# Kernel tuning notes

Measured on AMD Instinct MI355X. Metric: run time of the kernel, lower is better.

## Reference

```python
import jax, jax.numpy as jnp
import numpy as np

NUM_CLASSES = 40
EOS_COEF = 0.1
IGNORE = 255
W_CLASS, W_MASK, W_DICE = 2.0, 5.0, 5.0
EPS = 1e-8


def setup_inputs() -> dict:
    key = jax.random.key(0)
    k1, k2, k3, k4 = jax.random.split(key, 4)
    B, Q, H, W = 4, 100, 256, 256
    pred_logits = jax.random.normal(k1, (B, Q, NUM_CLASSES + 1), dtype=jnp.float32)
    pred_masks = jax.random.normal(k2, (B, Q, H, W), dtype=jnp.float32)
    targets = jax.random.randint(k3, (B, H, W), 0, NUM_CLASSES)
    ign = jax.random.uniform(k4, (B, H, W)) < 0.05
    targets = jnp.where(ign, IGNORE, targets).astype(jnp.int32)
    return {"pred_logits": pred_logits, "pred_masks": pred_masks, "targets": targets}


def reference(pred_logits, pred_masks, targets):
    B, Q, _ = pred_logits.shape
    C = NUM_CLASSES
    f32 = jnp.float32
    valid = targets != IGNORE                      # [B,H,W]
    tgt_safe = jnp.where(valid, targets, 0)        # in-range for indexing

    # ---- loss_labels: pixel->query assignment, per-query mode label ----
    # sigmoid is monotone, so argmax over queries of raw logits == argmax of sigmoid
    assign = jnp.argmax(pred_masks, axis=1)        # [B,H,W]
    b_idx = jnp.broadcast_to(jnp.arange(B)[:, None, None], targets.shape)
    # counts[b,q,c] = #valid pixels assigned to query q with label c
    counts = jnp.zeros((B, Q, C), f32).at[b_idx, assign, tgt_safe].add(valid.astype(f32))
    has_pix = counts.sum(-1) > 0                   # [B,Q]
    # mode = argmax of counts (ties -> smallest class, matching torch.mode)
    target_classes = jnp.where(has_pix, jnp.argmax(counts, axis=-1), C)  # [B,Q]

    logp = jax.nn.log_softmax(pred_logits, axis=-1)                      # [B,Q,C+1]
    nll = -jnp.take_along_axis(logp, target_classes[..., None], axis=-1)[..., 0]
    empty_weight = jnp.ones(C + 1, f32).at[-1].set(EOS_COEF)
    # ignore_index = num_classes in the CE over classes
    ce = jnp.where(target_classes != C, nll * empty_weight[target_classes], 0.0)
    p = jnp.exp(-ce)
    loss_ce = jnp.mean((1.0 - p) ** 2 * ce)

    # ---- loss_masks: per-pixel CE over queries + per-class dice ----
    logp_pix = jax.nn.log_softmax(pred_masks, axis=1)                    # [B,Q,H,W]
    nll_pix = -jnp.take_along_axis(logp_pix, tgt_safe[:, None], axis=1)[:, 0]  # [B,H,W]
    n_valid = valid.astype(f32).sum()
    ce_mask = jnp.sum(jnp.where(valid, nll_pix, 0.0)) / jnp.maximum(n_valid, 1.0)

    sig = jax.nn.sigmoid(pred_masks)                                     # [B,Q,H,W]
    tmask = (targets[:, None] == jnp.arange(C)[None, :, None, None]).astype(f32)  # [B,C,H,W]
    vm = valid[:, None].astype(f32)                                      # [B,1,H,W]
    inter = jnp.einsum('bqhw,bchw->bqc', sig, tmask * vm)                # numerator uses valid mask
    src_sum = sig.sum(axis=(2, 3))                                       # [B,Q]
    tsum = tmask.sum(axis=(2, 3))                                        # [B,C]
    dice = 2.0 * inter / (src_sum[:, :, None] + tsum[:, None, :] + EPS)  # [B,Q,C]
    present = tsum.sum(axis=0) > 0                                       # [C]
    dice_loss = jnp.sum(jnp.where(present, 1.0 - dice.mean(axis=(0, 1)), 0.0)) / C

    combined = W_MASK * ce_mask + W_DICE * dice_loss
    return W_CLASS * loss_ce + combined
```

## Files before the change

kernel.cpp:

```cpp
#include <hip/hip_runtime.h>
#include <hip/hip_bf16.h>

constexpr int B = 4, Q = 100, C = 40, Cp1 = 41, HW = 65536;
constexpr int NPIX = B * HW;

constexpr int APXT = 4, ATHR = 128;
constexpr int ABLK = NPIX / (APXT * ATHR);
constexpr int SLOT = ABLK / B;
constexpr int QU = 10;

constexpr int BTHR = 128, BCHUNKS = 8;
constexpr int BCPX = HW / BCHUNKS;
constexpr int BITERS = BCPX / (BTHR * 4);

constexpr int WS_WORDS = 32562;

__global__ void kZ(unsigned* __restrict__ ws, int n) {
    int i = blockIdx.x * blockDim.x + threadIdx.x;
    for (; i < n; i += gridDim.x * blockDim.x) ws[i] = 0u;
}

__global__ __launch_bounds__(ATHR) void kA(const float* __restrict__ masks,
                                           const int* __restrict__ targets,
                                           unsigned* __restrict__ counts,
                                           unsigned* __restrict__ tsum,
                                           float* __restrict__ ce_sum,
                                           unsigned* __restrict__ n_valid) {
    int tid = threadIdx.x;
    int blk = blockIdx.x;
    int b = blk / SLOT;
    int hw = (blk % SLOT) * (ATHR * APXT) + tid * APXT;
    const float* mp = masks + (size_t)b * Q * HW + hw;
    int4 tg = *(const int4*)(targets + (size_t)b * HW + hw);
    int tgs[4] = {tg.x, tg.y, tg.z, tg.w};

    float m[4] = {-INFINITY, -INFINITY, -INFINITY, -INFINITY};
    float s[4] = {0.f, 0.f, 0.f, 0.f};
    float xt[4] = {0.f, 0.f, 0.f, 0.f};
    int amax[4] = {0, 0, 0, 0};

    for (int qq = 0; qq < Q; qq += QU) {
        float4 vv[QU];
        #pragma unroll
        for (int u = 0; u < QU; ++u)
            vv[u] = *(const float4*)(mp + (size_t)(qq + u) * HW);
        #pragma unroll
        for (int u = 0; u < QU; ++u) {
            int q = qq + u;
            float v[4] = {vv[u].x, vv[u].y, vv[u].z, vv[u].w};
            #pragma unroll
            for (int j = 0; j < 4; ++j) {
                s[j] += __expf(v[j]);
                amax[j] = (v[j] > m[j]) ? q : amax[j];
                m[j] = fmaxf(m[j], v[j]);
                xt[j] = (q == tgs[j]) ? v[j] : xt[j];
            }
        }
    }

    __shared__ unsigned ts_local[C];
    __shared__ float cred[2];
    __shared__ unsigned vred[2];
    if (tid < C) ts_local[tid] = 0u;
    __syncthreads();

    float ce = 0.f;
    unsigned nv = 0;
    #pragma unroll
    for (int j = 0; j < 4; ++j) {
        if (tgs[j] != 255) {
            ce += __logf(s[j]) - xt[j];
            nv++;
            atomicAdd(&counts[((size_t)b * Q + amax[j]) * C + tgs[j]], 1u);
            atomicAdd(&ts_local[tgs[j]], 1u);
        }
    }

    for (int off = 32; off; off >>= 1) {
        ce += __shfl_xor(ce, off);
        nv += __shfl_xor(nv, off);
    }
    int lane = tid & 63, wave = tid >> 6;
    if (lane == 0) { cred[wave] = ce; vred[wave] = nv; }
    __syncthreads();
    if (tid == 0) {
        atomicAdd(ce_sum, cred[0] + cred[1]);
        atomicAdd(n_valid, vred[0] + vred[1]);
    }
    if (tid < C) {
        unsigned t = ts_local[tid];
        if (t) atomicAdd(&tsum[b * C + tid], t);
    }
}

__global__ __launch_bounds__(BTHR) void kB(const float* __restrict__ masks,
                                           const int* __restrict__ targets,
                                           float* __restrict__ inter,
                                           float* __restrict__ src_sum) {
    __shared__ float hist[C][BTHR];
    int tid = threadIdx.x;
    int bq = blockIdx.x >> 3;
    int chunk = blockIdx.x & 7;
    int b = bq / Q;
    const float* mp = masks + (size_t)bq * HW + chunk * BCPX;
    const int* tp = targets + (size_t)b * HW + chunk * BCPX;

    #pragma unroll
    for (int c = 0; c < C; ++c) hist[c][tid] = 0.f;

    float sacc = 0.f;
    #pragma unroll 4
    for (int it = 0; it < BITERS; ++it) {
        int off = it * (BTHR * 4) + tid * 4;
        float4 x = *(const float4*)(mp + off);
        int4 tg = *(const int4*)(tp + off);
        float xs[4] = {x.x, x.y, x.z, x.w};
        int cs[4] = {tg.x, tg.y, tg.z, tg.w};
        #pragma unroll
        for (int j = 0; j < 4; ++j) {
            float sig = __builtin_amdgcn_rcpf(1.f + __expf(-xs[j]));
            sacc += sig;
            if ((unsigned)cs[j] < (unsigned)C) hist[cs[j]][tid] += sig;
        }
    }

    for (int off = 32; off; off >>= 1) sacc += __shfl_xor(sacc, off);
    int lane = tid & 63, wave = tid >> 6;
    if (lane == 0) atomicAdd(&src_sum[bq], sacc);

    __syncthreads();
    for (int c = wave * 20; c < wave * 20 + 20; ++c) {
        float h = hist[c][lane] + hist[c][lane + 64];
        for (int off = 32; off; off >>= 1) h += __shfl_xor(h, off);
        if (lane == 0) atomicAdd(&inter[(size_t)bq * C + c], h);
    }
}

__global__ __launch_bounds__(512) void kC(const float* __restrict__ logits,
                                          const unsigned* __restrict__ counts,
                                          const unsigned* __restrict__ tsum,
                                          const float* __restrict__ inter,
                                          const float* __restrict__ src_sum,
                                          const float* __restrict__ ce_sum,
                                          const unsigned* __restrict__ n_valid,
                                          float* __restrict__ out) {
    int tid = threadIdx.x;
    __shared__ float dice_sum[C];
    __shared__ float wred[8];
    __shared__ float s_lce;
    if (tid < C) dice_sum[tid] = 0.f;

    float ce_acc = 0.f;
    for (int i = tid; i < B * Q; i += 512) {
        const unsigned* cnt = counts + (size_t)i * C;
        unsigned best = 0;
        int tc = C;
        #pragma unroll
        for (int c = 0; c < C; ++c) {
            unsigned v = cnt[c];
            if (v > best) { best = v; tc = c; }
        }
        if (tc != C) {
            const float* lg = logits + (size_t)i * Cp1;
            float mm = -INFINITY, xt = 0.f;
            #pragma unroll
            for (int c = 0; c < Cp1; ++c) {
                float v = lg[c];
                mm = fmaxf(mm, v);
                if (c == tc) xt = v;
            }
            float ss = 0.f;
            #pragma unroll
            for (int c = 0; c < Cp1; ++c) ss += __expf(lg[c] - mm);
            float nll = mm + __logf(ss) - xt;
            float p = __expf(-nll);
            float om = 1.f - p;
            ce_acc += om * om * nll;
        }
    }
    for (int off = 32; off; off >>= 1) ce_acc += __shfl_xor(ce_acc, off);
    if ((tid & 63) == 0) wred[tid >> 6] = ce_acc;
    __syncthreads();
    if (tid == 0) {
        float t = 0.f;
        for (int w = 0; w < 8; ++w) t += wred[w];
        s_lce = t;
    }

    for (int i = tid; i < B * Q * C; i += 512) {
        int bq = i / C, c = i - bq * C;
        float denom = src_sum[bq] + (float)tsum[(bq / Q) * C + c] + 1e-8f;
        atomicAdd(&dice_sum[c], 2.f * inter[i] / denom);
    }
    __syncthreads();

    if (tid == 0) {
        float dl = 0.f;
        for (int c = 0; c < C; ++c) {
            unsigned ts = tsum[c] + tsum[C + c] + tsum[2 * C + c] + tsum[3 * C + c];
            if (ts > 0) dl += 1.f - dice_sum[c] * (1.f / (B * Q));
        }
        dl *= (1.f / C);
        float ce_mask = ce_sum[0] / fmaxf((float)n_valid[0], 1.f);
        float lce = s_lce * (1.f / (B * Q));
        out[0] = 2.f * lce + 5.f * ce_mask + 5.f * dl;
    }
}

extern "C" void kernel_launch(void* const* d_in, const int* in_sizes, int n_in,
                              void* d_out, int out_size, void* d_ws, size_t ws_size,
                              hipStream_t stream) {
    const float* logits  = (const float*)d_in[0];
    const float* masks   = (const float*)d_in[1];
    const int*   targets = (const int*)d_in[2];
    float* out = (float*)d_out;

    unsigned* ws      = (unsigned*)d_ws;
    unsigned* counts  = ws;
    unsigned* tsum    = ws + 16000;
    float*    inter   = (float*)(ws + 16160);
    float*    src_sum = (float*)(ws + 32160);
    float*    ce_sum  = (float*)(ws + 32560);
    unsigned* n_valid = ws + 32561;

    kZ<<<64, 256, 0, stream>>>(ws, WS_WORDS);
    kA<<<ABLK, ATHR, 0, stream>>>(masks, targets, counts, tsum, ce_sum, n_valid);
    kB<<<B * Q * BCHUNKS, BTHR, 0, stream>>>(masks, targets, inter, src_sum);
    kC<<<1, 512, 0, stream>>>(logits, counts, tsum, inter, src_sum, ce_sum, n_valid, out);
}
```

Before: 230.8 us.

## Merge argmax/CE and dice histogram passes into one heterogeneous-block kernel

```diff
diff --git a/kernel.cpp b/kernel.cpp
--- a/kernel.cpp
+++ b/kernel.cpp
@@ -4,14 +4,16 @@
 constexpr int B = 4, Q = 100, C = 40, Cp1 = 41, HW = 65536;
 constexpr int NPIX = B * HW;
 
-constexpr int APXT = 4, ATHR = 128;
-constexpr int ABLK = NPIX / (APXT * ATHR);
-constexpr int SLOT = ABLK / B;
-constexpr int QU = 10;
-
-constexpr int BTHR = 128, BCHUNKS = 8;
-constexpr int BCPX = HW / BCHUNKS;
-constexpr int BITERS = BCPX / (BTHR * 4);
+constexpr int ATHR = 256, APX = 2;
+constexpr int ABLKS = NPIX / (ATHR * APX);
+constexpr int ASLOT = HW / (ATHR * APX);
+constexpr int QU = 5;
+
+constexpr int BCH = 8;
+constexpr int BCPX = HW / BCH;
+constexpr int BIT = BCPX / (ATHR * 4);
+
+constexpr int GRID = ABLKS + B * Q * BCH;
 
 constexpr int WS_WORDS = 32562;
 
@@ -20,119 +22,117 @@
     for (; i < n; i += gridDim.x * blockDim.x) ws[i] = 0u;
 }
 
-__global__ __launch_bounds__(ATHR) void kA(const float* __restrict__ masks,
-                                           const int* __restrict__ targets,
-                                           unsigned* __restrict__ counts,
-                                           unsigned* __restrict__ tsum,
-                                           float* __restrict__ ce_sum,
-                                           unsigned* __restrict__ n_valid) {
+__global__ __launch_bounds__(256, 4) void kBig(const float* __restrict__ masks,
+                                               const int* __restrict__ targets,
+                                               unsigned* __restrict__ counts,
+                                               unsigned* __restrict__ tsum,
+                                               float* __restrict__ ce_sum,
+                                               unsigned* __restrict__ n_valid,
+                                               float* __restrict__ inter,
+                                               float* __restrict__ src_sum) {
+    __shared__ float hist[C][ATHR];
     int tid = threadIdx.x;
     int blk = blockIdx.x;
-    int b = blk / SLOT;
-    int hw = (blk % SLOT) * (ATHR * APXT) + tid * APXT;
-    const float* mp = masks + (size_t)b * Q * HW + hw;
-    int4 tg = *(const int4*)(targets + (size_t)b * HW + hw);
-    int tgs[4] = {tg.x, tg.y, tg.z, tg.w};
-
-    float m[4] = {-INFINITY, -INFINITY, -INFINITY, -INFINITY};
-    float s[4] = {0.f, 0.f, 0.f, 0.f};
-    float xt[4] = {0.f, 0.f, 0.f, 0.f};
-    int amax[4] = {0, 0, 0, 0};
-
-    for (int qq = 0; qq < Q; qq += QU) {
-        float4 vv[QU];
+
+    if (blk < ABLKS) {
+        unsigned* ts_local = (unsigned*)&hist[0][0];
+        float*    cred     = &hist[0][64];
+        unsigned* vred     = (unsigned*)&hist[0][72];
+
+        int b = blk / ASLOT;
+        int hw = (blk % ASLOT) * (ATHR * APX) + tid * APX;
+        const float* mp = masks + (size_t)b * Q * HW + hw;
+        int2 tg = *(const int2*)(targets + (size_t)b * HW + hw);
+        int tgs[2] = {tg.x, tg.y};
+
+        float m[2] = {-INFINITY, -INFINITY}, s[2] = {0.f, 0.f}, xt[2] = {0.f, 0.f};
+        int amax[2] = {0, 0};
+
+        for (int qq = 0; qq < Q; qq += QU) {
+            float2 vv[QU];
+            #pragma unroll
+            for (int u = 0; u < QU; ++u)
+                vv[u] = *(const float2*)(mp + (size_t)(qq + u) * HW);
+            #pragma unroll
+            for (int u = 0; u < QU; ++u) {
+                int q = qq + u;
+                float v[2] = {vv[u].x, vv[u].y};
+                #pragma unroll
+                for (int j = 0; j < 2; ++j) {
+                    s[j] += __expf(v[j]);
+                    amax[j] = (v[j] > m[j]) ? q : amax[j];
+                    m[j] = fmaxf(m[j], v[j]);
+                    xt[j] = (q == tgs[j]) ? v[j] : xt[j];
+                }
+            }
+        }
+
+        if (tid < C) ts_local[tid] = 0u;
+        __syncthreads();
+
+        float ce = 0.f;
+        unsigned nv = 0;
         #pragma unroll
-        for (int u = 0; u < QU; ++u)
-            vv[u] = *(const float4*)(mp + (size_t)(qq + u) * HW);
+        for (int j = 0; j < 2; ++j) {
+            if (tgs[j] != 255) {
+                ce += __logf(s[j]) - xt[j];
+                nv++;
+                atomicAdd(&counts[((size_t)b * Q + amax[j]) * C + tgs[j]], 1u);
+                atomicAdd(&ts_local[tgs[j]], 1u);
+            }
+        }
+        for (int off = 32; off; off >>= 1) {
+            ce += __shfl_xor(ce, off);
+            nv += __shfl_xor(nv, off);
+        }
+        int lane = tid & 63, wave = tid >> 6;
+        if (lane == 0) { cred[wave] = ce; vred[wave] = nv; }
+        __syncthreads();
+        if (tid == 0) {
+            atomicAdd(ce_sum, cred[0] + cred[1] + cred[2] + cred[3]);
+            atomicAdd(n_valid, vred[0] + vred[1] + vred[2] + vred[3]);
+        }
+        if (tid < C) {
+            unsigned t = ts_local[tid];
+            if (t) atomicAdd(&tsum[b * C + tid], t);
+        }
+    } else {
+        int r = blk - ABLKS;
+        int bq = r >> 3;
+        int chunk = r & 7;
+        int b = bq / Q;
+        const float* mp = masks + (size_t)bq * HW + chunk * BCPX;
+        const int* tp = targets + (size_t)b * HW + chunk * BCPX;
+
         #pragma unroll
-        for (int u = 0; u < QU; ++u) {
-            int q = qq + u;
-            float v[4] = {vv[u].x, vv[u].y, vv[u].z, vv[u].w};
+        for (int c = 0; c < C; ++c) hist[c][tid] = 0.f;
+
+        float sacc = 0.f;
+        #pragma unroll 2
+        for (int it = 0; it < BIT; ++it) {
+            int off = it * (ATHR * 4) + tid * 4;
+            float4 x = *(const float4*)(mp + off);
+            int4 tg = *(const int4*)(tp + off);
+            float xs[4] = {x.x, x.y, x.z, x.w};
+            int cs[4] = {tg.x, tg.y, tg.z, tg.w};
             #pragma unroll
             for (int j = 0; j < 4; ++j) {
-                s[j] += __expf(v[j]);
-                amax[j] = (v[j] > m[j]) ? q : amax[j];
-                m[j] = fmaxf(m[j], v[j]);
-                xt[j] = (q == tgs[j]) ? v[j] : xt[j];
-            }
-        }
-    }
-
-    __shared__ unsigned ts_local[C];
-    __shared__ float cred[2];
-    __shared__ unsigned vred[2];
-    if (tid < C) ts_local[tid] = 0u;
-    __syncthreads();
-
-    float ce = 0.f;
-    unsigned nv = 0;
-    #pragma unroll
-    for (int j = 0; j < 4; ++j) {
-        if (tgs[j] != 255) {
-            ce += __logf(s[j]) - xt[j];
-            nv++;
-            atomicAdd(&counts[((size_t)b * Q + amax[j]) * C + tgs[j]], 1u);
-            atomicAdd(&ts_local[tgs[j]], 1u);
-        }
-    }
-
-    for (int off = 32; off; off >>= 1) {
-        ce += __shfl_xor(ce, off);
-        nv += __shfl_xor(nv, off);
-    }
-    int lane = tid & 63, wave = tid >> 6;
-    if (lane == 0) { cred[wave] = ce; vred[wave] = nv; }
-    __syncthreads();
-    if (tid == 0) {
-        atomicAdd(ce_sum, cred[0] + cred[1]);
-        atomicAdd(n_valid, vred[0] + vred[1]);
-    }
-    if (tid < C) {
-        unsigned t = ts_local[tid];
-        if (t) atomicAdd(&tsum[b * C + tid], t);
-    }
-}
-
-__global__ __launch_bounds__(BTHR) void kB(const float* __restrict__ masks,
-                                           const int* __restrict__ targets,
-                                           float* __restrict__ inter,
-                                           float* __restrict__ src_sum) {
-    __shared__ float hist[C][BTHR];
-    int tid = threadIdx.x;
-    int bq = blockIdx.x >> 3;
-    int chunk = blockIdx.x & 7;
-    int b = bq / Q;
-    const float* mp = masks + (size_t)bq * HW + chunk * BCPX;
-    const int* tp = targets + (size_t)b * HW + chunk * BCPX;
-
-    #pragma unroll
-    for (int c = 0; c < C; ++c) hist[c][tid] = 0.f;
-
-    float sacc = 0.f;
-    #pragma unroll 4
-    for (int it = 0; it < BITERS; ++it) {
-        int off = it * (BTHR * 4) + tid * 4;
-        float4 x = *(const float4*)(mp + off);
-        int4 tg = *(const int4*)(tp + off);
-        float xs[4] = {x.x, x.y, x.z, x.w};
-        int cs[4] = {tg.x, tg.y, tg.z, tg.w};
-        #pragma unroll
-        for (int j = 0; j < 4; ++j) {
-            float sig = __builtin_amdgcn_rcpf(1.f + __expf(-xs[j]));
-            sacc += sig;
-            if ((unsigned)cs[j] < (unsigned)C) hist[cs[j]][tid] += sig;
-        }
-    }
-
-    for (int off = 32; off; off >>= 1) sacc += __shfl_xor(sacc, off);
-    int lane = tid & 63, wave = tid >> 6;
-    if (lane == 0) atomicAdd(&src_sum[bq], sacc);
-
-    __syncthreads();
-    for (int c = wave * 20; c < wave * 20 + 20; ++c) {
-        float h = hist[c][lane] + hist[c][lane + 64];
-        for (int off = 32; off; off >>= 1) h += __shfl_xor(h, off);
-        if (lane == 0) atomicAdd(&inter[(size_t)bq * C + c], h);
+                float sig = 1.f / (1.f + __expf(-xs[j]));
+                sacc += sig;
+                if ((unsigned)cs[j] < (unsigned)C) hist[cs[j]][tid] += sig;
+            }
+        }
+
+        for (int off = 32; off; off >>= 1) sacc += __shfl_xor(sacc, off);
+        int lane = tid & 63, wave = tid >> 6;
+        if (lane == 0) atomicAdd(&src_sum[bq], sacc);
+
+        __syncthreads();
+        for (int c = wave * 10; c < wave * 10 + 10; ++c) {
+            float h = hist[c][lane] + hist[c][lane + 64] + hist[c][lane + 128] + hist[c][lane + 192];
+            for (int off = 32; off; off >>= 1) h += __shfl_xor(h, off);
+            if (lane == 0) atomicAdd(&inter[(size_t)bq * C + c], h);
+        }
     }
 }
 
@@ -224,7 +224,7 @@
     unsigned* n_valid = ws + 32561;
 
     kZ<<<64, 256, 0, stream>>>(ws, WS_WORDS);
-    kA<<<ABLK, ATHR, 0, stream>>>(masks, targets, counts, tsum, ce_sum, n_valid);
-    kB<<<B * Q * BCHUNKS, BTHR, 0, stream>>>(masks, targets, inter, src_sum);
+    kBig<<<GRID, ATHR, 0, stream>>>(masks, targets, counts, tsum, ce_sum, n_valid,
+                                    inter, src_sum);
     kC<<<1, 512, 0, stream>>>(logits, counts, tsum, inter, src_sum, ce_sum, n_valid, out);
 }
```

New measurement: 226.7 us. Within noise of the previous version (-1.8%).
